# Performance work log

Hardware: AMD Instinct MI355X
Metric: run time of the kernel (lower is better)

The kernel has to match this reference:

```python
import jax, jax.numpy as jnp
import numpy as np


def setup_inputs() -> dict:
    key = jax.random.key(0)
    k1, k2 = jax.random.split(key)
    A, B, N, M, K = 8, 16, 1024, 1024, 64
    u = jax.random.normal(k1, (A, B, N, K), dtype=jnp.float32)
    v = jax.random.normal(k2, (A, B, M, K), dtype=jnp.float32)
    return {"u": u, "v": v}


def reference(u, v):
    # to_norm = u @ v^T has shape (A,B,N,M); we only need its row/col sums.
    # sum over M of (u @ v^T) = u @ sum_m(v);  sum over N = v @ sum_n(u).
    v_sum = v.sum(axis=2)                     # (A,B,K)
    u_sum = u.sum(axis=2)                     # (A,B,K)
    row_sum = jnp.einsum('abnk,abk->abn', u, v_sum)   # to_norm.sum(dim=3)
    col_sum = jnp.einsum('abmk,abk->abm', v, u_sum)   # to_norm.sum(dim=2)
    left_mul = jax.nn.relu(jnp.sign(row_sum))[..., None]   # (A,B,N,1)
    right_mul = jax.nn.relu(jnp.sign(col_sum))[..., None]  # (A,B,M,1)
    return (left_mul * u, right_mul * v)
```

## Files before the change

### kernel.cpp

```cpp
#include <hip/hip_runtime.h>


#define NBATCH 128
#define NROW   1024
#define KDIM   64
#define NPART  4
#define ELEMS_PER_TENSOR (128ull * 1024ull * 64ull)

__global__ void sums_kernel(const float* __restrict__ u,
                            const float* __restrict__ v,
                            float* __restrict__ sums) {
    int bid    = blockIdx.x;
    int batch  = bid >> 2;
    int part   = bid & 3;
    int rstart = part * 256;
    int tid = threadIdx.x;
    int k4  = tid & 15;
    int rg  = tid >> 4;

    const float4* ub = (const float4*)(u + ((size_t)batch * NROW + rstart) * KDIM);
    const float4* vb = (const float4*)(v + ((size_t)batch * NROW + rstart) * KDIM);

    float4 su = make_float4(0.f, 0.f, 0.f, 0.f);
    float4 sv = make_float4(0.f, 0.f, 0.f, 0.f);
    #pragma unroll 4
    for (int i = 0; i < 16; ++i) {
        int r = rg + 16 * i;
        float4 a = ub[r * 16 + k4];
        float4 b = vb[r * 16 + k4];
        su.x += a.x; su.y += a.y; su.z += a.z; su.w += a.w;
        sv.x += b.x; sv.y += b.y; sv.z += b.z; sv.w += b.w;
    }

    __shared__ float4 lu[16][16];
    __shared__ float4 lv[16][16];
    lu[rg][k4] = su;
    lv[rg][k4] = sv;
    __syncthreads();

    if (tid < 32) {
        int which = tid >> 4;
        int c     = tid & 15;
        float4 t = make_float4(0.f, 0.f, 0.f, 0.f);
        if (which == 0) {
            #pragma unroll
            for (int i = 0; i < 16; ++i) {
                float4 b = lv[i][c];
                t.x += b.x; t.y += b.y; t.z += b.z; t.w += b.w;
            }
        } else {
            #pragma unroll
            for (int i = 0; i < 16; ++i) {
                float4 a = lu[i][c];
                t.x += a.x; t.y += a.y; t.z += a.z; t.w += a.w;
            }
        }
        float* dst = sums + (((size_t)(batch * NPART + part) * 2 + which) * KDIM) + c * 4;
        *(float4*)dst = t;
    }
}

__global__ void mask_kernel(const float* __restrict__ u,
                            const float* __restrict__ v,
                            const float* __restrict__ sums,
                            float* __restrict__ out) {
    int bid  = blockIdx.x;
    int is_v = bid >> 13;
    int lb   = bid & 8191;
    const float* src = is_v ? v : u;
    float* dst = out + (size_t)is_v * ELEMS_PER_TENSOR;

    int batch = lb >> 6;
    int row0  = (lb & 63) * 16;
    int tid   = threadIdx.x;

    __shared__ float s_lds[KDIM];
    if (tid < KDIM) {
        const float* p0 = sums + ((size_t)(batch * NPART) * 2 + is_v) * KDIM + tid;
        s_lds[tid] = p0[0] + p0[2 * KDIM] + p0[4 * KDIM] + p0[6 * KDIM];
    }
    __syncthreads();

    int k4 = tid & 15;
    int r  = row0 + (tid >> 4);

    size_t off = ((size_t)batch * NROW + r) * KDIM + (size_t)k4 * 4;
    float4 x   = *(const float4*)(src + off);
    float4 sv4 = *(const float4*)(s_lds + k4 * 4);

    float p = x.x * sv4.x + x.y * sv4.y + x.z * sv4.z + x.w * sv4.w;
    p += __shfl_xor(p, 1);
    p += __shfl_xor(p, 2);
    p += __shfl_xor(p, 4);
    p += __shfl_xor(p, 8);

    float m = (p > 0.f) ? 1.f : 0.f;
    float4 o = make_float4(x.x * m, x.y * m, x.z * m, x.w * m);
    *(float4*)(dst + off) = o;
}

extern "C" void kernel_launch(void* const* d_in, const int* in_sizes, int n_in,
                              void* d_out, int out_size, void* d_ws, size_t ws_size,
                              hipStream_t stream) {
    const float* u = (const float*)d_in[0];
    const float* v = (const float*)d_in[1];
    float* out  = (float*)d_out;
    float* sums = (float*)d_ws;

    sums_kernel<<<dim3(512), dim3(256), 0, stream>>>(u, v, sums);
    mask_kernel<<<dim3(16384), dim3(256), 0, stream>>>(u, v, sums, out);
}
```

Measured before the change: 120.5 us.

## Fuse sum and mask kernels into one cooperative kernel with register-held inputs

Merges the two-pass sums and mask kernels into a single cooperative launch of 256 blocks of 1024 threads, one block per half-batch. Each thread keeps its 8 rows of u and v in registers, writes partial sums, waits at a grid-wide sync, then computes the masks and writes the outputs without re-reading the inputs. This removes the second global read of u and v and one kernel launch. In exchange it depends on all 256 blocks being co-resident for the grid sync, adds grid-barrier cost, and uses enough registers per thread that occupancy may be low.

New measurement: 157.7 us. 1.31x slower.

```diff
diff --git a/kernel.cpp b/kernel.cpp
--- a/kernel.cpp
+++ b/kernel.cpp
@@ -1,102 +1,102 @@
 #include <hip/hip_runtime.h>
+#include <hip/hip_cooperative_groups.h>
+
+namespace cg = cooperative_groups;
 
 
 #define NBATCH 128
 #define NROW   1024
 #define KDIM   64
-#define NPART  4
 #define ELEMS_PER_TENSOR (128ull * 1024ull * 64ull)
 
-__global__ void sums_kernel(const float* __restrict__ u,
-                            const float* __restrict__ v,
-                            float* __restrict__ sums) {
-    int bid    = blockIdx.x;
-    int batch  = bid >> 2;
-    int part   = bid & 3;
-    int rstart = part * 256;
-    int tid = threadIdx.x;
-    int k4  = tid & 15;
-    int rg  = tid >> 4;
+#define WS_OFF(b, h, w) ((((size_t)(b) * 2 + (h)) * 2 + (w)) * KDIM)
 
-    const float4* ub = (const float4*)(u + ((size_t)batch * NROW + rstart) * KDIM);
-    const float4* vb = (const float4*)(v + ((size_t)batch * NROW + rstart) * KDIM);
+__global__ __launch_bounds__(1024, 4)
+void fused_kernel(const float* __restrict__ u,
+                  const float* __restrict__ v,
+                  float* __restrict__ out,
+                  float* __restrict__ ws) {
+    const int bid   = blockIdx.x;
+    const int batch = bid >> 1;
+    const int half  = bid & 1;
+    const int tid   = threadIdx.x;
+    const int k4    = tid & 15;
+    const int rg    = tid >> 4;
 
+    const size_t base_row = (size_t)batch * NROW + (size_t)half * 512;
+    const float4* ub = (const float4*)(u + base_row * KDIM);
+    const float4* vb = (const float4*)(v + base_row * KDIM);
+
+    float4 ur[8], vr[8];
     float4 su = make_float4(0.f, 0.f, 0.f, 0.f);
     float4 sv = make_float4(0.f, 0.f, 0.f, 0.f);
-    #pragma unroll 4
-    for (int i = 0; i < 16; ++i) {
-        int r = rg + 16 * i;
-        float4 a = ub[r * 16 + k4];
-        float4 b = vb[r * 16 + k4];
-        su.x += a.x; su.y += a.y; su.z += a.z; su.w += a.w;
-        sv.x += b.x; sv.y += b.y; sv.z += b.z; sv.w += b.w;
+    #pragma unroll
+    for (int i = 0; i < 8; ++i) {
+        size_t idx = (size_t)(rg + 64 * i) * 16 + k4;
+        ur[i] = ub[idx];
+        vr[i] = vb[idx];
+        su.x += ur[i].x; su.y += ur[i].y; su.z += ur[i].z; su.w += ur[i].w;
+        sv.x += vr[i].x; sv.y += vr[i].y; sv.z += vr[i].z; sv.w += vr[i].w;
     }
 
-    __shared__ float4 lu[16][16];
-    __shared__ float4 lv[16][16];
+    __shared__ float4 lu[64][16];
+    __shared__ float4 lv[64][16];
     lu[rg][k4] = su;
     lv[rg][k4] = sv;
     __syncthreads();
 
     if (tid < 32) {
-        int which = tid >> 4;
-        int c     = tid & 15;
+        const int which = tid >> 4;
+        const int c     = tid & 15;
         float4 t = make_float4(0.f, 0.f, 0.f, 0.f);
         if (which == 0) {
             #pragma unroll
-            for (int i = 0; i < 16; ++i) {
+            for (int i = 0; i < 64; ++i) {
                 float4 b = lv[i][c];
                 t.x += b.x; t.y += b.y; t.z += b.z; t.w += b.w;
             }
         } else {
             #pragma unroll
-            for (int i = 0; i < 16; ++i) {
+            for (int i = 0; i < 64; ++i) {
                 float4 a = lu[i][c];
                 t.x += a.x; t.y += a.y; t.z += a.z; t.w += a.w;
             }
         }
-        float* dst = sums + (((size_t)(batch * NPART + part) * 2 + which) * KDIM) + c * 4;
-        *(float4*)dst = t;
+        *(float4*)(ws + WS_OFF(batch, half, which) + c * 4) = t;
     }
-}
 
-__global__ void mask_kernel(const float* __restrict__ u,
-                            const float* __restrict__ v,
-                            const float* __restrict__ sums,
-                            float* __restrict__ out) {
-    int bid  = blockIdx.x;
-    int is_v = bid >> 13;
-    int lb   = bid & 8191;
-    const float* src = is_v ? v : u;
-    float* dst = out + (size_t)is_v * ELEMS_PER_TENSOR;
+    cg::this_grid().sync();
 
-    int batch = lb >> 6;
-    int row0  = (lb & 63) * 16;
-    int tid   = threadIdx.x;
+    float4 p0 = *(const float4*)(ws + WS_OFF(batch, 0, 0) + k4 * 4);
+    float4 p1 = *(const float4*)(ws + WS_OFF(batch, 1, 0) + k4 * 4);
+    float4 q0 = *(const float4*)(ws + WS_OFF(batch, 0, 1) + k4 * 4);
+    float4 q1 = *(const float4*)(ws + WS_OFF(batch, 1, 1) + k4 * 4);
+    float4 vsum = make_float4(p0.x + p1.x, p0.y + p1.y, p0.z + p1.z, p0.w + p1.w);
+    float4 usum = make_float4(q0.x + q1.x, q0.y + q1.y, q0.z + q1.z, q0.w + q1.w);
 
-    __shared__ float s_lds[KDIM];
-    if (tid < KDIM) {
-        const float* p0 = sums + ((size_t)(batch * NPART) * 2 + is_v) * KDIM + tid;
-        s_lds[tid] = p0[0] + p0[2 * KDIM] + p0[4 * KDIM] + p0[6 * KDIM];
+    float4* ou = (float4*)(out + base_row * KDIM);
+    float4* ov = (float4*)(out + ELEMS_PER_TENSOR + base_row * KDIM);
+
+    #pragma unroll
+    for (int i = 0; i < 8; ++i) {
+        size_t idx = (size_t)(rg + 64 * i) * 16 + k4;
+
+        float pu = ur[i].x * vsum.x + ur[i].y * vsum.y + ur[i].z * vsum.z + ur[i].w * vsum.w;
+        pu += __shfl_xor(pu, 1);
+        pu += __shfl_xor(pu, 2);
+        pu += __shfl_xor(pu, 4);
+        pu += __shfl_xor(pu, 8);
+        float mu = (pu > 0.f) ? 1.f : 0.f;
+        ou[idx] = make_float4(ur[i].x * mu, ur[i].y * mu, ur[i].z * mu, ur[i].w * mu);
+
+        float pv = vr[i].x * usum.x + vr[i].y * usum.y + vr[i].z * usum.z + vr[i].w * usum.w;
+        pv += __shfl_xor(pv, 1);
+        pv += __shfl_xor(pv, 2);
+        pv += __shfl_xor(pv, 4);
+        pv += __shfl_xor(pv, 8);
+        float mv = (pv > 0.f) ? 1.f : 0.f;
+        ov[idx] = make_float4(vr[i].x * mv, vr[i].y * mv, vr[i].z * mv, vr[i].w * mv);
     }
-    __syncthreads();
-
-    int k4 = tid & 15;
-    int r  = row0 + (tid >> 4);
-
-    size_t off = ((size_t)batch * NROW + r) * KDIM + (size_t)k4 * 4;
-    float4 x   = *(const float4*)(src + off);
-    float4 sv4 = *(const float4*)(s_lds + k4 * 4);
-
-    float p = x.x * sv4.x + x.y * sv4.y + x.z * sv4.z + x.w * sv4.w;
-    p += __shfl_xor(p, 1);
-    p += __shfl_xor(p, 2);
-    p += __shfl_xor(p, 4);
-    p += __shfl_xor(p, 8);
-
-    float m = (p > 0.f) ? 1.f : 0.f;
-    float4 o = make_float4(x.x * m, x.y * m, x.z * m, x.w * m);
-    *(float4*)(dst + off) = o;
 }
 
 extern "C" void kernel_launch(void* const* d_in, const int* in_sizes, int n_in,
@@ -104,9 +104,10 @@
                               hipStream_t stream) {
     const float* u = (const float*)d_in[0];
     const float* v = (const float*)d_in[1];
-    float* out  = (float*)d_out;
-    float* sums = (float*)d_ws;
+    float* out = (float*)d_out;
+    float* ws  = (float*)d_ws;
 
-    sums_kernel<<<dim3(512), dim3(256), 0, stream>>>(u, v, sums);
-    mask_kernel<<<dim3(16384), dim3(256), 0, stream>>>(u, v, sums, out);
+    void* args[] = {(void*)&u, (void*)&v, (void*)&out, (void*)&ws};
+    hipLaunchCooperativeKernel((void*)fused_kernel, dim3(256), dim3(1024),
+                               args, 0, stream);
 }
```
